# Kernel tuning notes

Hardware: AMD Instinct MI355X
Metric: run time of the kernel (lower is better)

Reference implementation:

```python
import jax, jax.numpy as jnp
import numpy as np

N = 50000
E = 800000
IN_DIM = 128
OUT_DIM = 128
EDGE_DIM = 3
H = 4
HD = OUT_DIM // H  # 32
SCALE = HD ** -0.5


def setup_inputs() -> dict:
    key = jax.random.key(0)
    ks = jax.random.split(key, 10)
    x = jax.random.normal(ks[0], (N, IN_DIM), dtype=jnp.float32)
    edge_index = jax.random.randint(ks[1], (2, E), 0, N, dtype=jnp.int64)
    edge_attr = jax.random.normal(ks[2], (E, EDGE_DIM), dtype=jnp.float32)
    s = 1.0 / np.sqrt(IN_DIM)
    Wq = jax.random.normal(ks[3], (IN_DIM, H * HD), dtype=jnp.float32) * s
    Wk = jax.random.normal(ks[4], (IN_DIM, H * HD), dtype=jnp.float32) * s
    Wv = jax.random.normal(ks[5], (IN_DIM, H * HD), dtype=jnp.float32) * s
    We = jax.random.normal(ks[6], (EDGE_DIM, H), dtype=jnp.float32) * (1.0 / np.sqrt(EDGE_DIM))
    Wo = jax.random.normal(ks[7], (H * HD, OUT_DIM), dtype=jnp.float32) * (1.0 / np.sqrt(H * HD))
    bo = jnp.zeros((OUT_DIM,), dtype=jnp.float32)
    Wm = jax.random.normal(ks[8], (IN_DIM + OUT_DIM, OUT_DIM), dtype=jnp.float32) * (1.0 / np.sqrt(IN_DIM + OUT_DIM))
    bm = jnp.zeros((OUT_DIM,), dtype=jnp.float32)
    return {"x": x, "edge_index": edge_index, "edge_attr": edge_attr,
            "Wq": Wq, "Wk": Wk, "Wv": Wv, "We": We, "Wo": Wo, "bo": bo,
            "Wm": Wm, "bm": bm}


def reference(x, edge_index, edge_attr, Wq, Wk, Wv, We, Wo, bo, Wm, bm):
    n = x.shape[0]
    src = edge_index[0]
    dst = edge_index[1]
    Q = (x @ Wq).reshape(n, H, HD)
    K = (x @ Wk).reshape(n, H, HD)
    V = (x @ Wv).reshape(n, H, HD)
    edge_bias = edge_attr @ We                                  # [E, H]
    attn = jnp.sum(Q[dst] * K[src], axis=-1) * SCALE + edge_bias  # [E, H]
    attn = jnp.where(attn >= 0, attn, 0.2 * attn)               # leaky_relu(0.2)
    # NOTE: original uses a single GLOBAL max over all edges/heads for stability
    attn_exp = jnp.exp(attn - jnp.max(attn))
    attn_sum = jax.ops.segment_sum(attn_exp, dst, num_segments=n)  # [N, H]
    attn_norm = attn_exp / jnp.maximum(attn_sum[dst], 1e-12)
    # dropout disabled (eval mode)
    weighted_V = V[src] * attn_norm[:, :, None]                 # [E, H, HD]
    agg = jax.ops.segment_sum(weighted_V, dst, num_segments=n)  # [N, H, HD]
    agg = agg.reshape(n, H * HD) @ Wo + bo                      # [N, OUT]
    h = jnp.concatenate([x, agg], axis=1) @ Wm + bm
    return jax.nn.relu(h)
```

## Files before the change

### kernel.cpp

```cpp
#include <hip/hip_runtime.h>
#include <hip/hip_bf16.h>
#include <math.h>

#define NN 50000
#define NE 800000
#define DIM 128
#define NH 4
#define HD 32
#define ATTN_SCALE 0.17677669529663687f
#define MTILE 64
#define GEMM_BLOCKS 782
#define NBKT 98
#define PTS 2048
#define HBLKS 104

#define PREP_QKV_BASE  104
#define PREP_WXB_BASE  296
#define PREP_X_BASE    361
#define PREP_GRID      6611

#define PART_N      391
#define PART_GRID   519

#define CSR_N       782
#define CSRQ_GRID   1564

typedef unsigned int uint;
typedef unsigned short ushort;
typedef __attribute__((ext_vector_type(8))) short short8;
typedef __attribute__((ext_vector_type(4))) float f32x4;

__device__ inline ushort f2bf(float f) {
    __hip_bfloat16 h = __float2bfloat16(f);
    return *(ushort*)&h;
}
__device__ inline float bflo(uint u) { return __uint_as_float(u << 16); }
__device__ inline float bfhi(uint u) { return __uint_as_float(u & 0xffff0000u); }
__device__ inline float bf2f(ushort u) { return __uint_as_float((uint)u << 16); }

__global__ __launch_bounds__(256) void prep_all_kernel(
    const float* __restrict__ x, ushort* __restrict__ xb,
    const int* __restrict__ dst, int* __restrict__ bkt_cnt,
    const float* __restrict__ Wq, const float* __restrict__ Wk,
    const float* __restrict__ Wv, short* __restrict__ BpQKV,
    const float* __restrict__ Wo, const float* __restrict__ Wm,
    const float* __restrict__ bo, const float* __restrict__ bm,
    float* __restrict__ Wx, float* __restrict__ bprime)
{
    const int bid = blockIdx.x;
    const int tid = threadIdx.x;

    if (bid < PREP_QKV_BASE) {
        __shared__ int c[NBKT];
        if (tid < NBKT) c[tid] = 0;
        __syncthreads();
        for (int e = bid * 256 + tid; e < NE; e += HBLKS * 256)
            atomicAdd(&c[dst[e] >> 9], 1);
        __syncthreads();
        if (tid < NBKT && c[tid]) atomicAdd(&bkt_cnt[tid], c[tid]);
    } else if (bid < PREP_WXB_BASE) {
        const int idx = (bid - PREP_QKV_BASE) * 256 + tid;
        const int j = idx & 7, lane = (idx >> 3) & 63;
        const int rest = idx >> 9;
        const int nt = rest % 24, kc = rest / 24;
        const int k = kc * 32 + (lane >> 4) * 8 + j;
        const int n = nt * 16 + (lane & 15);
        const float* W = (n < 128) ? Wq : (n < 256 ? Wk : Wv);
        BpQKV[idx] = (short)f2bf(W[k * 128 + (n & 127)]);
    } else if (bid < PREP_X_BASE) {
        const int r = (bid - PREP_WXB_BASE) * 2 + (tid >> 7);
        const int j = tid & 127;
        if (r < 128) {
            float acc = 0.f;
            for (int t = 0; t < 128; ++t)
                acc = fmaf(Wo[r * 128 + t], Wm[(128 + t) * 128 + j], acc);
            Wx[r * 128 + j] = acc;
        } else if (r == 128) {
            float acc = bm[j];
            for (int t = 0; t < 128; ++t)
                acc = fmaf(bo[t], Wm[(128 + t) * 128 + j], acc);
            bprime[j] = acc;
        }
    } else {
        const int i = (bid - PREP_X_BASE) * 256 + tid;
        const float4 v = ((const float4*)x)[i];
        ushort4 o;
        o.x = f2bf(v.x); o.y = f2bf(v.y); o.z = f2bf(v.z); o.w = f2bf(v.w);
        ((ushort4*)xb)[i] = o;
    }
}

__global__ void bkt_scan_kernel(const int* __restrict__ bkt_cnt,
                                int* __restrict__ bkt_base,
                                int* __restrict__ bkt_cursor,
                                int* __restrict__ rowptr)
{
    if (threadIdx.x == 0) {
        int run = 0;
        for (int b = 0; b < NBKT; ++b) {
            bkt_base[b] = run;
            bkt_cursor[b] = run;
            run += bkt_cnt[b];
        }
        bkt_base[NBKT] = run;
        rowptr[NN] = run;
    }
}

__global__ __launch_bounds__(256) void part_kernel(
    const int* __restrict__ src, const int* __restrict__ dst,
    const float* __restrict__ edge_attr, const float* __restrict__ We,
    int* __restrict__ bkt_cursor,
    uint* __restrict__ ppack, uint2* __restrict__ pebp,
    const float* __restrict__ Wm, const float* __restrict__ Wx,
    short* __restrict__ BpOut)
{
    const int bid = blockIdx.x;
    const int tid = threadIdx.x;

    if (bid < PART_N) {
        __shared__ int cnt[NBKT], rbase[NBKT], cnt2[NBKT];
        if (tid < NBKT) cnt[tid] = 0;
        __syncthreads();
        const int e0 = bid * PTS;
        #pragma unroll
        for (int it = 0; it < 8; ++it) {
            const int e = e0 + it * 256 + tid;
            if (e < NE) atomicAdd(&cnt[dst[e] >> 9], 1);
        }
        __syncthreads();
        if (tid < NBKT) {
            rbase[tid] = cnt[tid] ? atomicAdd(&bkt_cursor[tid], cnt[tid]) : 0;
            cnt2[tid] = 0;
        }
        __syncthreads();
        #pragma unroll
        for (int it = 0; it < 8; ++it) {
            const int e = e0 + it * 256 + tid;
            if (e < NE) {
                const int d = dst[e];
                const int b = d >> 9;
                const int r = atomicAdd(&cnt2[b], 1);
                const int pos = rbase[b] + r;
                ppack[pos] = (uint)src[e] | ((uint)(d & 511) << 16);
                const float a0 = edge_attr[e * 3 + 0];
                const float a1 = edge_attr[e * 3 + 1];
                const float a2 = edge_attr[e * 3 + 2];
                const float b0 = a0 * We[0] + a1 * We[4] + a2 * We[8];
                const float b1 = a0 * We[1] + a1 * We[5] + a2 * We[9];
                const float b2 = a0 * We[2] + a1 * We[6] + a2 * We[10];
                const float b3 = a0 * We[3] + a1 * We[7] + a2 * We[11];
                uint2 ep;
                ep.x = (uint)f2bf(b0) | ((uint)f2bf(b1) << 16);
                ep.y = (uint)f2bf(b2) | ((uint)f2bf(b3) << 16);
                pebp[pos] = ep;
            }
        }
    } else {
        const int idx = (bid - PART_N) * 256 + tid;
        const int j = idx & 7, lane = (idx >> 3) & 63;
        const int rest = idx >> 9;
        const int nt = rest & 7, kc = rest >> 3;
        const int k = kc * 32 + (lane >> 4) * 8 + j;
        const int n = nt * 16 + (lane & 15);
        const float v = (k < 128) ? Wm[k * 128 + n] : Wx[(k - 128) * 128 + n];
        BpOut[idx] = (short)f2bf(v);
    }
}

__global__ __launch_bounds__(256) void csrqkv_kernel(
    const int* __restrict__ bkt_base,
    const uint* __restrict__ ppack, const uint2* __restrict__ pebp,
    int* __restrict__ rowptr,
    ushort* __restrict__ srcp, uint2* __restrict__ ebq,
    const ushort* __restrict__ xb, const short* __restrict__ BpQKV,
    ushort* __restrict__ Qb, ushort* __restrict__ KVb)
{
    const int bid = blockIdx.x;
    const int tid = threadIdx.x;

    if (bid < CSR_N) {
        __shared__ int cnt[512];
        __shared__ int pre[512];
        __shared__ int sc[256];
        const int parent = bid >> 3;
        const int sub    = bid & 7;
        const int base = bkt_base[parent];
        const int n = bkt_base[parent + 1] - base;
        const int node0 = parent << 9;

        cnt[tid] = 0; cnt[tid + 256] = 0;
        __syncthreads();
        for (int i = base + tid; i < base + n; i += 256)
            atomicAdd(&cnt[ppack[i] >> 16], 1);
        __syncthreads();

        const int pair = cnt[2 * tid] + cnt[2 * tid + 1];
        sc[tid] = pair;
        __syncthreads();
        for (int off = 1; off < 256; off <<= 1) {
            const int v = (tid >= off) ? sc[tid - off] : 0;
            __syncthreads();
            sc[tid] += v;
            __syncthreads();
        }
        const int ex = sc[tid] - pair;
        pre[2 * tid] = base + ex;
        pre[2 * tid + 1] = base + ex + cnt[2 * tid];
        __syncthreads();

        if (tid < 64) {
            const int l = sub * 64 + tid;
            const int g = node0 + l;
            if (g < NN) rowptr[g] = pre[l];
        }
        __syncthreads();

        for (int i = base + tid; i < base + n; i += 256) {
            const uint v = ppack[i];
            const int l = v >> 16;
            if ((l >> 6) == sub) {
                const int pos = atomicAdd(&pre[l], 1);
                srcp[pos] = (ushort)(v & 0xFFFFu);
                ebq[pos] = pebp[i];
            }
        }
    } else {
        const int qb = bid - CSR_N;
        const int wave = tid >> 6;
        const int lane = tid & 63;
        const int m = lane & 15, quad = lane >> 4;
        const int row0w = qb * MTILE + wave * 16;
        const int arow = row0w + m;
        const bool rowok = arow < NN;

        short8 a[4];
        #pragma unroll
        for (int kc = 0; kc < 4; ++kc)
            a[kc] = rowok ? *(const short8*)(xb + (size_t)arow * 128 + kc * 32 + quad * 8)
                          : (short8)(0);

        const int NT = 24;
        for (int nt = 0; nt < NT; nt += 2) {
            f32x4 acc0 = {0.f, 0.f, 0.f, 0.f}, acc1 = {0.f, 0.f, 0.f, 0.f};
            #pragma unroll
            for (int kc = 0; kc < 4; ++kc) {
                const short8 b0 = *(const short8*)(BpQKV + ((size_t)(kc * NT + nt) * 64 + lane) * 8);
                const short8 b1 = *(const short8*)(BpQKV + ((size_t)(kc * NT + nt + 1) * 64 + lane) * 8);
                acc0 = __builtin_amdgcn_mfma_f32_16x16x32_bf16(a[kc], b0, acc0, 0, 0, 0);
                acc1 = __builtin_amdgcn_mfma_f32_16x16x32_bf16(a[kc], b1, acc1, 0, 0, 0);
            }
            #pragma unroll
            for (int t = 0; t < 2; ++t) {
                const f32x4 acc = t ? acc1 : acc0;
                const int c = (nt + t) * 16 + m;
                #pragma unroll
                for (int g = 0; g < 4; ++g) {
                    const int r = row0w + quad * 4 + g;
                    if (r < NN) {
                        if (c < 128) Qb[(size_t)r * 128 + c] = f2bf(acc[g]);
                        else        KVb[(size_t)r * 256 + (c - 128)] = f2bf(acc[g]);
                    }
                }
            }
        }
    }
}

__global__ __launch_bounds__(256) void out_mfma_kernel(
    const ushort* __restrict__ xb, const ushort* __restrict__ aggb,
    const short* __restrict__ Bp, const float* __restrict__ bprime,
    float* __restrict__ out)
{
    const int wave = threadIdx.x >> 6;
    const int lane = threadIdx.x & 63;
    const int m = lane & 15, quad = lane >> 4;
    const int row0w = blockIdx.x * MTILE + wave * 16;
    const int arow = row0w + m;
    const bool rowok = arow < NN;

    short8 a[8];
    #pragma unroll
    for (int kc = 0; kc < 4; ++kc)
        a[kc] = rowok ? *(const short8*)(xb + (size_t)arow * 128 + kc * 32 + quad * 8)
                      : (short8)(0);
    #pragma unroll
    for (int kc = 0; kc < 4; ++kc)
        a[4 + kc] = rowok ? *(const short8*)(aggb + (size_t)arow * 128 + kc * 32 + quad * 8)
                          : (short8)(0);

    const int NT = 8;
    for (int nt = 0; nt < NT; nt += 2) {
        f32x4 acc0 = {0.f, 0.f, 0.f, 0.f}, acc1 = {0.f, 0.f, 0.f, 0.f};
        #pragma unroll
        for (int kc = 0; kc < 8; ++kc) {
            const short8 b0 = *(const short8*)(Bp + ((size_t)(kc * NT + nt) * 64 + lane) * 8);
            const short8 b1 = *(const short8*)(Bp + ((size_t)(kc * NT + nt + 1) * 64 + lane) * 8);
            acc0 = __builtin_amdgcn_mfma_f32_16x16x32_bf16(a[kc], b0, acc0, 0, 0, 0);
            acc1 = __builtin_amdgcn_mfma_f32_16x16x32_bf16(a[kc], b1, acc1, 0, 0, 0);
        }
        #pragma unroll
        for (int t = 0; t < 2; ++t) {
            const f32x4 acc = t ? acc1 : acc0;
            const int c = (nt + t) * 16 + m;
            const float bb = bprime[c];
            #pragma unroll
            for (int g = 0; g < 4; ++g) {
                const int r = row0w + quad * 4 + g;
                if (r < NN) out[(size_t)r * 128 + c] = fmaxf(acc[g] + bb, 0.f);
            }
        }
    }
}

__global__ __launch_bounds__(256) void attn_agg_kernel(
    const ushort* __restrict__ Qb, const ushort* __restrict__ KVb,
    const int* __restrict__ rowptr, const ushort* __restrict__ srcp,
    const ushort* __restrict__ ebb, ushort* __restrict__ aggb)
{
    const int tid = threadIdx.x;
    const int d = blockIdx.x * 4 + (tid >> 6);
    const int lane = tid & 63;
    const int g = lane >> 4;
    const int t = lane & 15;
    const int h = t >> 2;
    const int begin = rowptr[d];
    const int end   = rowptr[d + 1];

    const uint4 uq = *(const uint4*)(Qb + (size_t)d * DIM + 8 * t);
    const float q0 = bflo(uq.x), q1 = bfhi(uq.x);
    const float q2 = bflo(uq.y), q3 = bfhi(uq.y);
    const float q4 = bflo(uq.z), q5 = bfhi(uq.z);
    const float q6 = bflo(uq.w), q7 = bfhi(uq.w);

    float ss = 0.f;
    float a0 = 0.f, a1 = 0.f, a2 = 0.f, a3 = 0.f;
    float a4 = 0.f, a5 = 0.f, a6 = 0.f, a7 = 0.f;

    if (begin < end) {
        int ec = begin + g;
        if (ec >= end) ec = end - 1;
        int s    = (int)srcp[ec];
        float eb = bf2f(ebb[ec * 4 + h]);

        for (int p = begin; p < end; p += 4) {
            const bool ok = (p + g) < end;
            const int pn = p + 4;
            int sn = s; float ebn = eb;
            if (pn < end) {
                int en = pn + g;
                if (en >= end) en = end - 1;
                sn  = (int)srcp[en];
                ebn = bf2f(ebb[en * 4 + h]);
            }

            const ushort* kv = KVb + (size_t)s * 256 + 8 * t;
            const uint4 uk = *(const uint4*)(kv);
            const uint4 uv = *(const uint4*)(kv + 128);

            float da = q0 * bflo(uk.x);
            float db = q1 * bfhi(uk.x);
            da = fmaf(q2, bflo(uk.y), da);
            db = fmaf(q3, bfhi(uk.y), db);
            da = fmaf(q4, bflo(uk.z), da);
            db = fmaf(q5, bfhi(uk.z), db);
            da = fmaf(q6, bflo(uk.w), da);
            db = fmaf(q7, bfhi(uk.w), db);
            float part = da + db;
            part += __shfl_xor(part, 1);
            part += __shfl_xor(part, 2);

            float a = fmaf(part, ATTN_SCALE, eb);
            a = (a >= 0.f) ? a : 0.2f * a;
            float w = ok ? __expf(a) : 0.f;

            ss += w;
            a0 = fmaf(w, bflo(uv.x), a0);
            a1 = fmaf(w, bfhi(uv.x), a1);
            a2 = fmaf(w, bflo(uv.y), a2);
            a3 = fmaf(w, bfhi(uv.y), a3);
            a4 = fmaf(w, bflo(uv.z), a4);
            a5 = fmaf(w, bfhi(uv.z), a5);
            a6 = fmaf(w, bflo(uv.w), a6);
            a7 = fmaf(w, bfhi(uv.w), a7);

            s = sn; eb = ebn;
        }
    }

    ss += __shfl_xor(ss, 16);
    ss += __shfl_xor(ss, 32);
    a0 += __shfl_xor(a0, 16); a0 += __shfl_xor(a0, 32);
    a1 += __shfl_xor(a1, 16); a1 += __shfl_xor(a1, 32);
    a2 += __shfl_xor(a2, 16); a2 += __shfl_xor(a2, 32);
    a3 += __shfl_xor(a3, 16); a3 += __shfl_xor(a3, 32);
    a4 += __shfl_xor(a4, 16); a4 += __shfl_xor(a4, 32);
    a5 += __shfl_xor(a5, 16); a5 += __shfl_xor(a5, 32);
    a6 += __shfl_xor(a6, 16); a6 += __shfl_xor(a6, 32);
    a7 += __shfl_xor(a7, 16); a7 += __shfl_xor(a7, 32);

    if (g == 0) {
        const float inv = 1.f / fmaxf(ss, 1e-12f);
        uint4 o;
        o.x = (uint)f2bf(a0 * inv) | ((uint)f2bf(a1 * inv) << 16);
        o.y = (uint)f2bf(a2 * inv) | ((uint)f2bf(a3 * inv) << 16);
        o.z = (uint)f2bf(a4 * inv) | ((uint)f2bf(a5 * inv) << 16);
        o.w = (uint)f2bf(a6 * inv) | ((uint)f2bf(a7 * inv) << 16);
        *(uint4*)(aggb + (size_t)d * DIM + 8 * t) = o;
    }
}

extern "C" void kernel_launch(void* const* d_in, const int* in_sizes, int n_in,
                              void* d_out, int out_size, void* d_ws, size_t ws_size,
                              hipStream_t stream)
{
    const float* x         = (const float*)d_in[0];
    const int*   edge_idx  = (const int*)d_in[1];
    const float* edge_attr = (const float*)d_in[2];
    const float* Wq        = (const float*)d_in[3];
    const float* Wk        = (const float*)d_in[4];
    const float* Wv        = (const float*)d_in[5];
    const float* We        = (const float*)d_in[6];
    const float* Wo        = (const float*)d_in[7];
    const float* bo        = (const float*)d_in[8];
    const float* Wm        = (const float*)d_in[9];
    const float* bm        = (const float*)d_in[10];
    float* out = (float*)d_out;

    const int* src = edge_idx;
    const int* dst = edge_idx + NE;

    ushort* xb   = (ushort*)d_ws;
    ushort* Qb   = xb + (size_t)NN * DIM;
    ushort* KVb  = Qb + (size_t)NN * DIM;
    ushort* aggb = KVb + (size_t)NN * 2 * DIM;
    uint*  ppack = (uint*)(aggb + (size_t)NN * DIM);
    uint2* pebp  = (uint2*)(ppack + NE);
    uint2* ebq   = pebp + NE;
    ushort* srcp = (ushort*)(ebq + NE);
    float* Wx    = (float*)(srcp + NE);
    float* bprime= Wx + 16384;
    short* BpQKV = (short*)(bprime + 128);
    short* BpOut = BpQKV + 49152;
    int*   rowptr= (int*)(BpOut + 32768);
    int*   bkt_cnt    = rowptr + 50048;
    int*   bkt_base   = bkt_cnt + 128;
    int*   bkt_cursor = bkt_base + 128;

    hipMemsetAsync(bkt_cnt, 0, 128 * sizeof(int), stream);

    prep_all_kernel<<<PREP_GRID, 256, 0, stream>>>(
        x, xb, dst, bkt_cnt, Wq, Wk, Wv, BpQKV, Wo, Wm, bo, bm, Wx, bprime);

    bkt_scan_kernel<<<1, 64, 0, stream>>>(bkt_cnt, bkt_base, bkt_cursor, rowptr);

    part_kernel<<<PART_GRID, 256, 0, stream>>>(
        src, dst, edge_attr, We, bkt_cursor, ppack, pebp, Wm, Wx, BpOut);

    csrqkv_kernel<<<CSRQ_GRID, 256, 0, stream>>>(
        bkt_base, ppack, pebp, rowptr, srcp, ebq, xb, BpQKV, Qb, KVb);

    attn_agg_kernel<<<NN / 4, 256, 0, stream>>>(Qb, KVb, rowptr, srcp,
                                                (const ushort*)ebq, aggb);

    out_mfma_kernel<<<GEMM_BLOCKS, 256, 0, stream>>>(xb, aggb, BpOut, bprime, out);
}
```

Measured before the change: 249.3 us.

## Use 64-node buckets for CSR build and move x conversion into partition kernel

Bucket granularity for the edge partition changes from 512-node buckets (98) to 64-node buckets (782). Each CSR block now handles exactly one bucket, so it no longer rescans the 512-node bucket eight times and filters by sub-range, and the block-wide prefix scan becomes a single-wave shuffle scan. The bucket scan kernel becomes a parallel 256-thread scan, and the x-to-bf16 conversion moves from the first kernel into the partition kernel. In exchange the shared-memory histograms grow and there are more global cursor atomics per partition block.

```diff
diff --git a/kernel.cpp b/kernel.cpp
--- a/kernel.cpp
+++ b/kernel.cpp
@@ -10,20 +10,19 @@
 #define ATTN_SCALE 0.17677669529663687f
 #define MTILE 64
 #define GEMM_BLOCKS 782
-#define NBKT 98
+#define NBK 782
 #define PTS 2048
 #define HBLKS 104
 
-#define PREP_QKV_BASE  104
-#define PREP_WXB_BASE  296
-#define PREP_X_BASE    361
-#define PREP_GRID      6611
-
-#define PART_N      391
-#define PART_GRID   519
-
-#define CSR_N       782
-#define CSRQ_GRID   1564
+#define K1_QKV_BASE 104
+#define K1_WXB_BASE 296
+#define K1_GRID     361
+#define K3_PART_N     391
+#define K3_PACKO_BASE 391
+#define K3_XCVT_BASE  519
+#define K3_GRID       6769
+#define K4_CSR_N 782
+#define K4_GRID  1564
 
 typedef unsigned int uint;
 typedef unsigned short ushort;
@@ -38,8 +37,7 @@
 __device__ inline float bfhi(uint u) { return __uint_as_float(u & 0xffff0000u); }
 __device__ inline float bf2f(ushort u) { return __uint_as_float((uint)u << 16); }
 
-__global__ __launch_bounds__(256) void prep_all_kernel(
-    const float* __restrict__ x, ushort* __restrict__ xb,
+__global__ __launch_bounds__(256) void k1_kernel(
     const int* __restrict__ dst, int* __restrict__ bkt_cnt,
     const float* __restrict__ Wq, const float* __restrict__ Wk,
     const float* __restrict__ Wv, short* __restrict__ BpQKV,
@@ -50,16 +48,17 @@
     const int bid = blockIdx.x;
     const int tid = threadIdx.x;
 
-    if (bid < PREP_QKV_BASE) {
-        __shared__ int c[NBKT];
-        if (tid < NBKT) c[tid] = 0;
+    if (bid < HBLKS) {
+        __shared__ int c[NBK];
+        for (int l = tid; l < NBK; l += 256) c[l] = 0;
         __syncthreads();
         for (int e = bid * 256 + tid; e < NE; e += HBLKS * 256)
-            atomicAdd(&c[dst[e] >> 9], 1);
-        __syncthreads();
-        if (tid < NBKT && c[tid]) atomicAdd(&bkt_cnt[tid], c[tid]);
-    } else if (bid < PREP_WXB_BASE) {
-        const int idx = (bid - PREP_QKV_BASE) * 256 + tid;
+            atomicAdd(&c[dst[e] >> 6], 1);
+        __syncthreads();
+        for (int l = tid; l < NBK; l += 256)
+            if (c[l]) atomicAdd(&bkt_cnt[l], c[l]);
+    } else if (bid < K1_WXB_BASE) {
+        const int idx = (bid - K1_QKV_BASE) * 256 + tid;
         const int j = idx & 7, lane = (idx >> 3) & 63;
         const int rest = idx >> 9;
         const int nt = rest % 24, kc = rest / 24;
@@ -67,8 +66,8 @@
         const int n = nt * 16 + (lane & 15);
         const float* W = (n < 128) ? Wq : (n < 256 ? Wk : Wv);
         BpQKV[idx] = (short)f2bf(W[k * 128 + (n & 127)]);
-    } else if (bid < PREP_X_BASE) {
-        const int r = (bid - PREP_WXB_BASE) * 2 + (tid >> 7);
+    } else {
+        const int r = (bid - K1_WXB_BASE) * 2 + (tid >> 7);
         const int j = tid & 127;
         if (r < 128) {
             float acc = 0.f;
@@ -81,57 +80,68 @@
                 acc = fmaf(bo[t], Wm[(128 + t) * 128 + j], acc);
             bprime[j] = acc;
         }
-    } else {
-        const int i = (bid - PREP_X_BASE) * 256 + tid;
-        const float4 v = ((const float4*)x)[i];
-        ushort4 o;
-        o.x = f2bf(v.x); o.y = f2bf(v.y); o.z = f2bf(v.z); o.w = f2bf(v.w);
-        ((ushort4*)xb)[i] = o;
-    }
-}
-
-__global__ void bkt_scan_kernel(const int* __restrict__ bkt_cnt,
-                                int* __restrict__ bkt_base,
-                                int* __restrict__ bkt_cursor,
-                                int* __restrict__ rowptr)
-{
-    if (threadIdx.x == 0) {
-        int run = 0;
-        for (int b = 0; b < NBKT; ++b) {
-            bkt_base[b] = run;
-            bkt_cursor[b] = run;
-            run += bkt_cnt[b];
-        }
-        bkt_base[NBKT] = run;
-        rowptr[NN] = run;
-    }
-}
-
-__global__ __launch_bounds__(256) void part_kernel(
+    }
+}
+
+__global__ __launch_bounds__(256) void bkt_scan_kernel(
+    const int* __restrict__ bkt_cnt,
+    int* __restrict__ bkt_base, int* __restrict__ bkt_cursor,
+    int* __restrict__ rowptr)
+{
+    __shared__ int part[256];
+    const int tid = threadIdx.x;
+    const int b0 = tid * 4;
+    int v0 = 0, v1 = 0, v2 = 0, v3 = 0;
+    if (b0 + 0 < NBK) v0 = bkt_cnt[b0 + 0];
+    if (b0 + 1 < NBK) v1 = bkt_cnt[b0 + 1];
+    if (b0 + 2 < NBK) v2 = bkt_cnt[b0 + 2];
+    if (b0 + 3 < NBK) v3 = bkt_cnt[b0 + 3];
+    const int s = v0 + v1 + v2 + v3;
+    part[tid] = s;
+    __syncthreads();
+    for (int off = 1; off < 256; off <<= 1) {
+        const int y = (tid >= off) ? part[tid - off] : 0;
+        __syncthreads();
+        part[tid] += y;
+        __syncthreads();
+    }
+    const int ex = part[tid] - s;
+    const int r0 = ex, r1 = ex + v0, r2 = ex + v0 + v1, r3 = ex + v0 + v1 + v2;
+    if (b0 + 0 < NBK) { bkt_base[b0 + 0] = r0; bkt_cursor[b0 + 0] = r0; }
+    if (b0 + 1 < NBK) { bkt_base[b0 + 1] = r1; bkt_cursor[b0 + 1] = r1; }
+    if (b0 + 2 < NBK) { bkt_base[b0 + 2] = r2; bkt_cursor[b0 + 2] = r2; }
+    if (b0 + 3 < NBK) { bkt_base[b0 + 3] = r3; bkt_cursor[b0 + 3] = r3; }
+    if (tid == 255) bkt_base[NBK] = part[255];
+    if (tid == 0)   rowptr[NN] = NE;
+}
+
+__global__ __launch_bounds__(256) void k3_kernel(
     const int* __restrict__ src, const int* __restrict__ dst,
     const float* __restrict__ edge_attr, const float* __restrict__ We,
     int* __restrict__ bkt_cursor,
     uint* __restrict__ ppack, uint2* __restrict__ pebp,
     const float* __restrict__ Wm, const float* __restrict__ Wx,
-    short* __restrict__ BpOut)
+    short* __restrict__ BpOut,
+    const float* __restrict__ x, ushort* __restrict__ xb)
 {
     const int bid = blockIdx.x;
     const int tid = threadIdx.x;
 
-    if (bid < PART_N) {
-        __shared__ int cnt[NBKT], rbase[NBKT], cnt2[NBKT];
-        if (tid < NBKT) cnt[tid] = 0;
+    if (bid < K3_PART_N) {
+        __shared__ int cnt[NBK], rbase[NBK], cnt2[NBK];
+        for (int l = tid; l < NBK; l += 256) cnt[l] = 0;
         __syncthreads();
         const int e0 = bid * PTS;
         #pragma unroll
         for (int it = 0; it < 8; ++it) {
             const int e = e0 + it * 256 + tid;
-            if (e < NE) atomicAdd(&cnt[dst[e] >> 9], 1);
-        }
-        __syncthreads();
-        if (tid < NBKT) {
-            rbase[tid] = cnt[tid] ? atomicAdd(&bkt_cursor[tid], cnt[tid]) : 0;
-            cnt2[tid] = 0;
+            if (e < NE) atomicAdd(&cnt[dst[e] >> 6], 1);
+        }
+        __syncthreads();
+        for (int l = tid; l < NBK; l += 256) {
+            const int c = cnt[l];
+            rbase[l] = c ? atomicAdd(&bkt_cursor[l], c) : 0;
+            cnt2[l] = 0;
         }
         __syncthreads();
         #pragma unroll
@@ -139,10 +149,10 @@
             const int e = e0 + it * 256 + tid;
             if (e < NE) {
                 const int d = dst[e];
-                const int b = d >> 9;
+                const int b = d >> 6;
                 const int r = atomicAdd(&cnt2[b], 1);
                 const int pos = rbase[b] + r;
-                ppack[pos] = (uint)src[e] | ((uint)(d & 511) << 16);
+                ppack[pos] = (uint)src[e] | ((uint)(d & 63) << 16);
                 const float a0 = edge_attr[e * 3 + 0];
                 const float a1 = edge_attr[e * 3 + 1];
                 const float a2 = edge_attr[e * 3 + 2];
@@ -156,8 +166,8 @@
                 pebp[pos] = ep;
             }
         }
-    } else {
-        const int idx = (bid - PART_N) * 256 + tid;
+    } else if (bid < K3_XCVT_BASE) {
+        const int idx = (bid - K3_PACKO_BASE) * 256 + tid;
         const int j = idx & 7, lane = (idx >> 3) & 63;
         const int rest = idx >> 9;
         const int nt = rest & 7, kc = rest >> 3;
@@ -165,10 +175,16 @@
         const int n = nt * 16 + (lane & 15);
         const float v = (k < 128) ? Wm[k * 128 + n] : Wx[(k - 128) * 128 + n];
         BpOut[idx] = (short)f2bf(v);
-    }
-}
-
-__global__ __launch_bounds__(256) void csrqkv_kernel(
+    } else {
+        const int i = (bid - K3_XCVT_BASE) * 256 + tid;
+        const float4 v = ((const float4*)x)[i];
+        ushort4 o;
+        o.x = f2bf(v.x); o.y = f2bf(v.y); o.z = f2bf(v.z); o.w = f2bf(v.w);
+        ((ushort4*)xb)[i] = o;
+    }
+}
+
+__global__ __launch_bounds__(256) void k4_kernel(
     const int* __restrict__ bkt_base,
     const uint* __restrict__ ppack, const uint2* __restrict__ pebp,
     int* __restrict__ rowptr,
@@ -179,54 +195,42 @@
     const int bid = blockIdx.x;
     const int tid = threadIdx.x;
 
-    if (bid < CSR_N) {
-        __shared__ int cnt[512];
-        __shared__ int pre[512];
-        __shared__ int sc[256];
-        const int parent = bid >> 3;
-        const int sub    = bid & 7;
-        const int base = bkt_base[parent];
-        const int n = bkt_base[parent + 1] - base;
-        const int node0 = parent << 9;
-
-        cnt[tid] = 0; cnt[tid + 256] = 0;
+    if (bid < K4_CSR_N) {
+        __shared__ int cnt[64];
+        __shared__ int pre[64];
+        const int base = bkt_base[bid];
+        const int n = bkt_base[bid + 1] - base;
+        const int node0 = bid << 6;
+
+        if (tid < 64) cnt[tid] = 0;
         __syncthreads();
         for (int i = base + tid; i < base + n; i += 256)
             atomicAdd(&cnt[ppack[i] >> 16], 1);
         __syncthreads();
 
-        const int pair = cnt[2 * tid] + cnt[2 * tid + 1];
-        sc[tid] = pair;
-        __syncthreads();
-        for (int off = 1; off < 256; off <<= 1) {
-            const int v = (tid >= off) ? sc[tid - off] : 0;
-            __syncthreads();
-            sc[tid] += v;
-            __syncthreads();
-        }
-        const int ex = sc[tid] - pair;
-        pre[2 * tid] = base + ex;
-        pre[2 * tid + 1] = base + ex + cnt[2 * tid];
-        __syncthreads();
-
         if (tid < 64) {
-            const int l = sub * 64 + tid;
-            const int g = node0 + l;
-            if (g < NN) rowptr[g] = pre[l];
+            const int c = cnt[tid];
+            int xsc = c;
+            #pragma unroll
+            for (int off = 1; off < 64; off <<= 1) {
+                const int y = __shfl_up(xsc, off);
+                if (tid >= off) xsc += y;
+            }
+            const int ex = base + xsc - c;
+            pre[tid] = ex;
+            const int g = node0 + tid;
+            if (g < NN) rowptr[g] = ex;
         }
         __syncthreads();
 
         for (int i = base + tid; i < base + n; i += 256) {
             const uint v = ppack[i];
-            const int l = v >> 16;
-            if ((l >> 6) == sub) {
-                const int pos = atomicAdd(&pre[l], 1);
-                srcp[pos] = (ushort)(v & 0xFFFFu);
-                ebq[pos] = pebp[i];
-            }
+            const int pos = atomicAdd(&pre[v >> 16], 1);
+            srcp[pos] = (ushort)(v & 0xFFFFu);
+            ebq[pos] = pebp[i];
         }
     } else {
-        const int qb = bid - CSR_N;
+        const int qb = bid - K4_CSR_N;
         const int wave = tid >> 6;
         const int lane = tid & 63;
         const int m = lane & 15, quad = lane >> 4;
@@ -444,20 +448,20 @@
     short* BpOut = BpQKV + 49152;
     int*   rowptr= (int*)(BpOut + 32768);
     int*   bkt_cnt    = rowptr + 50048;
-    int*   bkt_base   = bkt_cnt + 128;
-    int*   bkt_cursor = bkt_base + 128;
-
-    hipMemsetAsync(bkt_cnt, 0, 128 * sizeof(int), stream);
-
-    prep_all_kernel<<<PREP_GRID, 256, 0, stream>>>(
-        x, xb, dst, bkt_cnt, Wq, Wk, Wv, BpQKV, Wo, Wm, bo, bm, Wx, bprime);
-
-    bkt_scan_kernel<<<1, 64, 0, stream>>>(bkt_cnt, bkt_base, bkt_cursor, rowptr);
-
-    part_kernel<<<PART_GRID, 256, 0, stream>>>(
-        src, dst, edge_attr, We, bkt_cursor, ppack, pebp, Wm, Wx, BpOut);
-
-    csrqkv_kernel<<<CSRQ_GRID, 256, 0, stream>>>(
+    int*   bkt_base   = bkt_cnt + 800;
+    int*   bkt_cursor = bkt_base + 800;
+
+    hipMemsetAsync(bkt_cnt, 0, NBK * sizeof(int), stream);
+
+    k1_kernel<<<K1_GRID, 256, 0, stream>>>(
+        dst, bkt_cnt, Wq, Wk, Wv, BpQKV, Wo, Wm, bo, bm, Wx, bprime);
+
+    bkt_scan_kernel<<<1, 256, 0, stream>>>(bkt_cnt, bkt_base, bkt_cursor, rowptr);
+
+    k3_kernel<<<K3_GRID, 256, 0, stream>>>(
+        src, dst, edge_attr, We, bkt_cursor, ppack, pebp, Wm, Wx, BpOut, x, xb);
+
+    k4_kernel<<<K4_GRID, 256, 0, stream>>>(
         bkt_base, ppack, pebp, rowptr, srcp, ebq, xb, BpQKV, Qb, KVb);
 
     attn_agg_kernel<<<NN / 4, 256, 0, stream>>>(Qb, KVb, rowptr, srcp,
```

Result: no change. 245.4 us (-1.6%).
